# Performance work log

Measured on AMD Instinct MI355X. Metric: run time of the kernel, lower is better.

Reference implementation:

```python
import jax, jax.numpy as jnp
import numpy as np

B, N, DIM_X, DIM_E = 16, 2048, 512, 64


def setup_inputs() -> dict:
    key = jax.random.key(0)
    kx, ke, k0, k1, k2, k3 = jax.random.split(key, 6)
    s = lambda fan_in: 1.0 / np.sqrt(fan_in)
    return {
        "x": jax.random.normal(kx, (B, N, DIM_X), dtype=jnp.float32),
        "e": jax.random.normal(ke, (N, DIM_E), dtype=jnp.float32),
        # nn.Linear weights: shape [out_features, in_features], U(-1/sqrt(in), 1/sqrt(in))
        "W0": jax.random.uniform(k0, (DIM_X, DIM_X), jnp.float32, -s(DIM_X), s(DIM_X)),  # W_Q_W_KT
        "W1": jax.random.uniform(k1, (DIM_E, DIM_X), jnp.float32, -s(DIM_X), s(DIM_X)),  # Wx_Q_We_KT
        "W2": jax.random.uniform(k2, (DIM_X, DIM_E), jnp.float32, -s(DIM_E), s(DIM_E)),  # We_Q_Wx_KT
        "W3": jax.random.uniform(k3, (DIM_E, DIM_E), jnp.float32, -s(DIM_E), s(DIM_E)),  # We_Q_We_KT
    }


def reference(x, e, W0, W1, W2, W3):
    # causal_temporal_map='lower_triangle': weight <- relu(triu(weight, 1))
    W0m = jax.nn.relu(jnp.triu(W0, 1))
    # attn0 = (x @ W0m.T) @ x^T over time axis t   -> [b, n, m]
    attn0 = jnp.einsum("bnt,bmt->bnm", x @ W0m.T, x)
    # e is shared across batch (repeat); keep it 2D and broadcast
    attn1 = jnp.einsum("bne,me->bnm", x @ W1.T, e)        # Wx_Q_We_KT(x) . e
    attn2 = jnp.einsum("nt,bmt->bnm", e @ W2.T, x)        # We_Q_Wx_KT(e) . x
    attn3 = jnp.einsum("ne,me->nm", e @ W3.T, e)          # We_Q_We_KT(e) . e, batch-shared
    attn = attn0 + attn1 + attn2 + attn3[None]            # dropout p=0.0 -> identity
    # v = x.clone(); out = attn @ v
    out = jnp.einsum("bnm,bmt->bnt", attn, x)
    return out
```

## Files before the change

### kernel.cpp

```cpp
#include <hip/hip_runtime.h>
#include <hip/hip_bf16.h>


typedef __attribute__((ext_vector_type(8))) short s16x8;
typedef __attribute__((ext_vector_type(4))) short s16x4;
typedef __attribute__((ext_vector_type(4))) float f32x4;

__device__ __forceinline__ unsigned short f2bf(float f) {
  union { float f; unsigned u; } v; v.f = f;
  unsigned r = v.u + 0x7fff + ((v.u >> 16) & 1);
  return (unsigned short)(r >> 16);
}

template<int TM, int TN, int GX, int GY, int OUT_F32>
__global__ __launch_bounds__(256) void gemm_nt(
    const unsigned short* __restrict__ A, long sAb, int lda,
    const unsigned short* __restrict__ B, long sBb, int ldb,
    void* __restrict__ Cptr, long sCb, int ldc,
    int K)
{
  constexpr int TK = 64;
  constexpr int WM = TM / 2, WN = TN / 2;
  constexpr int AM = WM / 16, AN = WN / 16;
  constexpr int ACH = TM / 8;
  constexpr int BCH = TN / 8;
  constexpr int NBLK = GX * GY;

  __shared__ unsigned short As[2][TM * TK];
  __shared__ unsigned short Bs[2][TN * TK];

  const int bid  = blockIdx.x;
  const int xcd  = bid & 7;
  const int slot = bid >> 3;
  const int bz   = xcd + 8 * (slot / NBLK);
  const int tix  = slot % NBLK;
  const int m0   = (tix % GX) * TM;
  const int n0   = (tix / GX) * TN;

  const unsigned short* Ab = A + (long)bz * sAb;
  const unsigned short* Bb = B + (long)bz * sBb;

  const int tid  = threadIdx.x;
  const int lane = tid & 63;
  const int wave = tid >> 6;
  const int wm = (wave >> 1) * WM;
  const int wn = (wave & 1) * WN;
  const int fr = lane & 15;
  const int fg = lane >> 4;
  const int fx = fr & 7;

  const int srow = lane >> 3;
  const int scol = (((lane & 7) ^ (lane >> 3)) & 7) * 8;

  f32x4 acc[AM][AN];
#pragma unroll
  for (int i = 0; i < AM; i++)
#pragma unroll
    for (int j = 0; j < AN; j++) acc[i][j] = (f32x4)(0.f);

  auto stage = [&](int buf, int k0) {
#pragma unroll
    for (int i = 0; i < ACH / 4; i++) {
      const int c = wave * (ACH / 4) + i;
      __builtin_amdgcn_global_load_lds(
          (const __attribute__((address_space(1))) unsigned*)
              (Ab + (long)(m0 + c * 8 + srow) * lda + k0 + scol),
          (__attribute__((address_space(3))) unsigned*)(&As[buf][c * 512]),
          16, 0, 0);
    }
#pragma unroll
    for (int i = 0; i < BCH / 4; i++) {
      const int c = wave * (BCH / 4) + i;
      __builtin_amdgcn_global_load_lds(
          (const __attribute__((address_space(1))) unsigned*)
              (Bb + (long)(n0 + c * 8 + srow) * ldb + k0 + scol),
          (__attribute__((address_space(3))) unsigned*)(&Bs[buf][c * 512]),
          16, 0, 0);
    }
  };

  const int NT = K / TK;
  stage(0, 0);
  __syncthreads();

  for (int t = 0; t < NT; ++t) {
    const int cur = t & 1;
    if (t + 1 < NT) stage(cur ^ 1, (t + 1) * TK);

    const unsigned short* Ac = &As[cur][0];
    const unsigned short* Bc = &Bs[cur][0];
#pragma unroll
    for (int ks = 0; ks < 2; ks++) {
      s16x8 av[AM], bv[AN];
#pragma unroll
      for (int mt = 0; mt < AM; mt++)
        av[mt] = *(const s16x8*)
            &Ac[(wm + mt * 16 + fr) * TK + (((ks * 4 + fg) ^ fx) * 8)];
#pragma unroll
      for (int nt = 0; nt < AN; nt++)
        bv[nt] = *(const s16x8*)
            &Bc[(wn + nt * 16 + fr) * TK + (((ks * 4 + fg) ^ fx) * 8)];
#pragma unroll
      for (int mt = 0; mt < AM; mt++)
#pragma unroll
        for (int nt = 0; nt < AN; nt++)
          acc[mt][nt] = __builtin_amdgcn_mfma_f32_16x16x32_bf16(
              av[mt], bv[nt], acc[mt][nt], 0, 0, 0);
    }
    __syncthreads();
  }

  if (OUT_F32) {
    float* C = (float*)Cptr + (long)bz * sCb;
#pragma unroll
    for (int mt = 0; mt < AM; mt++) {
      const int row = m0 + wm + mt * 16 + fg * 4;
#pragma unroll
      for (int nt = 0; nt < AN; nt++) {
        const int col = n0 + wn + nt * 16 + fr;
#pragma unroll
        for (int j = 0; j < 4; j++)
          C[(long)(row + j) * ldc + col] = acc[mt][nt][j];
      }
    }
  } else {
    unsigned short* C = (unsigned short*)Cptr + (long)bz * sCb;
#pragma unroll
    for (int mt = 0; mt < AM; mt++) {
      const int row = m0 + wm + mt * 16 + fg * 4;
#pragma unroll
      for (int nt = 0; nt < AN; nt++) {
        const int col = n0 + wn + nt * 16 + fr;
#pragma unroll
        for (int j = 0; j < 4; j++)
          C[(long)(row + j) * ldc + col] = f2bf(acc[mt][nt][j]);
      }
    }
  }
}

__global__ __launch_bounds__(256) void convert_x(
    const float* __restrict__ x,
    unsigned short* __restrict__ XeT, unsigned short* __restrict__ Xe)
{
  const int b  = blockIdx.z;
  const int k0 = blockIdx.x * 128;
  const int f0 = blockIdx.y * 128;
  const int lane = threadIdx.x & 63;
  const int w    = threadIdx.x >> 6;
  const int fg = lane & 15;
  const int kg = w * 4 + (lane >> 4);
  const int kk = k0 + kg * 8;
  const int ff = f0 + fg * 8;

  unsigned short h[8][8];
#pragma unroll
  for (int j = 0; j < 8; ++j) {
    const float* src = &x[((long)b * 2048 + kk + j) * 512 + ff];
    float4 a = *(const float4*)src;
    float4 c = *(const float4*)(src + 4);
    h[j][0] = f2bf(a.x); h[j][1] = f2bf(a.y);
    h[j][2] = f2bf(a.z); h[j][3] = f2bf(a.w);
    h[j][4] = f2bf(c.x); h[j][5] = f2bf(c.y);
    h[j][6] = f2bf(c.z); h[j][7] = f2bf(c.w);
  }
  if (Xe) {
#pragma unroll
    for (int j = 0; j < 8; ++j) {
      s16x8 o;
#pragma unroll
      for (int q = 0; q < 8; ++q) o[q] = h[j][q];
      *(s16x8*)&Xe[((long)b * 2048 + kk + j) * 576 + ff] = o;
    }
  }
#pragma unroll
  for (int r = 0; r < 8; ++r) {
    s16x8 o;
#pragma unroll
    for (int q = 0; q < 8; ++q) o[q] = h[q][r];
    *(s16x8*)&XeT[((long)b * 576 + ff + r) * 2048 + kk] = o;
  }
}

__global__ __launch_bounds__(256) void convert_e(
    const float* __restrict__ e,
    unsigned short* __restrict__ XeT, unsigned short* __restrict__ Xe)
{
  const int b  = blockIdx.y;
  const int k0 = blockIdx.x * 256;
  const int lane = threadIdx.x & 63;
  const int w    = threadIdx.x >> 6;
  const int fg = lane & 7;
  const int kg = w * 8 + (lane >> 3);
  const int kk = k0 + kg * 8;
  const int ff = fg * 8;

  unsigned short h[8][8];
#pragma unroll
  for (int j = 0; j < 8; ++j) {
    const float* src = &e[(long)(kk + j) * 64 + ff];
    float4 a = *(const float4*)src;
    float4 c = *(const float4*)(src + 4);
    h[j][0] = f2bf(a.x); h[j][1] = f2bf(a.y);
    h[j][2] = f2bf(a.z); h[j][3] = f2bf(a.w);
    h[j][4] = f2bf(c.x); h[j][5] = f2bf(c.y);
    h[j][6] = f2bf(c.z); h[j][7] = f2bf(c.w);
  }
  if (Xe) {
#pragma unroll
    for (int j = 0; j < 8; ++j) {
      s16x8 o;
#pragma unroll
      for (int q = 0; q < 8; ++q) o[q] = h[j][q];
      *(s16x8*)&Xe[((long)b * 2048 + kk + j) * 576 + 512 + ff] = o;
    }
  }
#pragma unroll
  for (int r = 0; r < 8; ++r) {
    s16x8 o;
#pragma unroll
    for (int q = 0; q < 8; ++q) o[q] = h[q][r];
    *(s16x8*)&XeT[((long)b * 576 + 512 + ff + r) * 2048 + kk] = o;
  }
}

__global__ __launch_bounds__(256) void convert_xe(
    const float* __restrict__ x, const float* __restrict__ e,
    unsigned short* __restrict__ Xe)
{
  long g = (long)blockIdx.x * 256 + threadIdx.x;
  int  c4 = (int)(g % 144);
  long bn = g / 144;
  int  n  = (int)(bn % 2048);
  int  f  = c4 * 4;
  float4 v = (f < 512) ? *(const float4*)&x[bn * 512 + f]
                       : *(const float4*)&e[(long)n * 64 + (f - 512)];
  s16x4 o; o[0] = f2bf(v.x); o[1] = f2bf(v.y); o[2] = f2bf(v.z); o[3] = f2bf(v.w);
  *(s16x4*)&Xe[bn * 576 + f] = o;
}

__global__ __launch_bounds__(256) void build_wb(
    const float* __restrict__ W0, const float* __restrict__ W1,
    const float* __restrict__ W2, const float* __restrict__ W3,
    unsigned short* __restrict__ Wb)
{
  __shared__ float tw[32][33];
  const int m0 = blockIdx.x * 32;
  const int k0 = blockIdx.y * 32;
  const int r  = threadIdx.x >> 3;
  const int c4 = (threadIdx.x & 7) * 4;

  const int k = k0 + r;
  float4 v;
  if (m0 < 512) {
    if (k0 < 512) v = *(const float4*)&W0[k * 512 + m0 + c4];
    else          v = *(const float4*)&W1[(k - 512) * 512 + m0 + c4];
  } else {
    if (k0 < 512) v = *(const float4*)&W2[k * 64 + (m0 - 512) + c4];
    else          v = *(const float4*)&W3[(k - 512) * 64 + (m0 - 512) + c4];
  }
  tw[r][c4 + 0] = v.x; tw[r][c4 + 1] = v.y; tw[r][c4 + 2] = v.z; tw[r][c4 + 3] = v.w;
  __syncthreads();

  const int m = m0 + r;
  const bool tri = (m0 < 512) && (k0 < 512);
  s16x4 o;
#pragma unroll
  for (int j = 0; j < 4; ++j) {
    const int kk = k0 + c4 + j;
    float val = tw[c4 + j][r];
    if (tri) val = (m > kk) ? fmaxf(val, 0.f) : 0.f;
    o[j] = f2bf(val);
  }
  *(s16x4*)&Wb[m * 576 + k0 + c4] = o;
}

extern "C" void kernel_launch(void* const* d_in, const int* in_sizes, int n_in,
                              void* d_out, int out_size, void* d_ws, size_t ws_size,
                              hipStream_t stream) {
  const float* x  = (const float*)d_in[0];
  const float* e  = (const float*)d_in[1];
  const float* W0 = (const float*)d_in[2];
  const float* W1 = (const float*)d_in[3];
  const float* W2 = (const float*)d_in[4];
  const float* W3 = (const float*)d_in[5];
  float* out = (float*)d_out;

  const size_t SZ_XeT = (size_t)16 * 576 * 2048 * 2;
  const size_t SZ_CT  = (size_t)16 * 512 * 576 * 2;
  const size_t SZ_DT  = SZ_CT;
  const size_t SZ_WB  = (size_t)576 * 576 * 2;

  char* p = (char*)d_ws;
  unsigned short* XeT = (unsigned short*)p;  p += SZ_XeT;
  unsigned short* CT  = (unsigned short*)p;  p += SZ_CT;
  unsigned short* DT  = (unsigned short*)p;  p += SZ_DT;
  unsigned short* Wb  = (unsigned short*)p;  p += SZ_WB;
  const size_t base = SZ_XeT + SZ_CT + SZ_DT + SZ_WB;
  if (ws_size < base) return;
  const bool roomy = ws_size >= base + SZ_XeT;
  unsigned short* Xe = roomy ? (unsigned short*)p : XeT;

  build_wb<<<dim3(18, 18), 256, 0, stream>>>(W0, W1, W2, W3, Wb);
  convert_x<<<dim3(16, 4, 16), 256, 0, stream>>>(x, XeT, roomy ? Xe : nullptr);
  convert_e<<<dim3(8, 16), 256, 0, stream>>>(e, XeT, roomy ? Xe : nullptr);

  gemm_nt<64, 96, 8, 6, 0><<<768, 256, 0, stream>>>(
      XeT, (long)576 * 2048, 2048,
      XeT, (long)576 * 2048, 2048,
      CT,  (long)512 * 576, 576, 2048);

  if (!roomy)
    convert_xe<<<18432, 256, 0, stream>>>(x, e, Xe);

  gemm_nt<64, 96, 8, 6, 0><<<768, 256, 0, stream>>>(
      CT, (long)512 * 576, 576,
      Wb, 0L, 576,
      DT, (long)512 * 576, 576, 576);

  gemm_nt<128, 128, 16, 4, 1><<<1024, 256, 0, stream>>>(
      Xe, (long)2048 * 576, 576,
      DT, (long)512 * 576, 576,
      out, (long)2048 * 512, 512, 576);
}
```

Measured before the change: 97.96 us.

## Exploit Gram-matrix symmetry in first GEMM and split x/e operands in final GEMM

The first GEMM now computes the full 576x576 Gram matrix of [x;e] over time, but only its lower-triangular 64x64 tiles, using a triangular block index. A new mirror kernel then copies the transposed lower tiles into the rows the next GEMM reads. The final GEMM no longer needs a concatenated 576-wide Xe buffer: it reads separate bf16 x and e buffers and switches source pointer partway through K. This cuts roughly a third of the largest GEMM's MMA work and removes the interleaved Xe copy, at the cost of an extra mirror launch and a serial loop for tile index decoding.

New measurement: 100.3 us. +2.4%, slower.

```diff
diff --git a/kernel.cpp b/kernel.cpp
--- a/kernel.cpp
+++ b/kernel.cpp
@@ -12,9 +12,10 @@
   return (unsigned short)(r >> 16);
 }
 
-template<int TM, int TN, int GX, int GY, int OUT_F32>
+template<int TM, int TN, int GX, int GY, int OUT_F32, int TRI, int KSW>
 __global__ __launch_bounds__(256) void gemm_nt(
     const unsigned short* __restrict__ A, long sAb, int lda,
+    const unsigned short* __restrict__ A2, int lda2,
     const unsigned short* __restrict__ B, long sBb, int ldb,
     void* __restrict__ Cptr, long sCb, int ldc,
     int K)
@@ -24,7 +25,7 @@
   constexpr int AM = WM / 16, AN = WN / 16;
   constexpr int ACH = TM / 8;
   constexpr int BCH = TN / 8;
-  constexpr int NBLK = GX * GY;
+  constexpr int NBLK = TRI ? (GX * (GX + 1)) / 2 : GX * GY;
 
   __shared__ unsigned short As[2][TM * TK];
   __shared__ unsigned short Bs[2][TN * TK];
@@ -34,8 +35,14 @@
   const int slot = bid >> 3;
   const int bz   = xcd + 8 * (slot / NBLK);
   const int tix  = slot % NBLK;
-  const int m0   = (tix % GX) * TM;
-  const int n0   = (tix / GX) * TN;
+  int m0, n0;
+  if (TRI) {
+    int ti = 0, rem = tix;
+    while (rem >= ti + 1) { rem -= ti + 1; ++ti; }
+    m0 = ti * TM; n0 = rem * TN;
+  } else {
+    m0 = (tix % GX) * TM; n0 = (tix / GX) * TN;
+  }
 
   const unsigned short* Ab = A + (long)bz * sAb;
   const unsigned short* Bb = B + (long)bz * sBb;
@@ -58,13 +65,18 @@
 #pragma unroll
     for (int j = 0; j < AN; j++) acc[i][j] = (f32x4)(0.f);
 
-  auto stage = [&](int buf, int k0) {
+  auto stage = [&](int buf, int t) {
+    const int k0 = t * TK;
+    const unsigned short* asrc;
+    int asl;
+    if (KSW >= 0 && t >= KSW) { asrc = A2 + (k0 - KSW * TK); asl = lda2; }
+    else                      { asrc = Ab + k0;              asl = lda;  }
 #pragma unroll
     for (int i = 0; i < ACH / 4; i++) {
       const int c = wave * (ACH / 4) + i;
       __builtin_amdgcn_global_load_lds(
           (const __attribute__((address_space(1))) unsigned*)
-              (Ab + (long)(m0 + c * 8 + srow) * lda + k0 + scol),
+              (asrc + (long)(m0 + c * 8 + srow) * asl + scol),
           (__attribute__((address_space(3))) unsigned*)(&As[buf][c * 512]),
           16, 0, 0);
     }
@@ -85,7 +97,7 @@
 
   for (int t = 0; t < NT; ++t) {
     const int cur = t & 1;
-    if (t + 1 < NT) stage(cur ^ 1, (t + 1) * TK);
+    if (t + 1 < NT) stage(cur ^ 1, t + 1);
 
     const unsigned short* Ac = &As[cur][0];
     const unsigned short* Bc = &Bs[cur][0];
@@ -139,9 +151,40 @@
   }
 }
 
+__global__ __launch_bounds__(256) void mirror_g(unsigned short* __restrict__ G)
+{
+  const int it = blockIdx.x;
+  const int jt = blockIdx.y;
+  if (jt < it) return;
+  const long S = (long)576 * 576;
+  unsigned short* Gb = G + (long)blockIdx.z * S;
+  const int i0 = it * 32, j0 = jt * 32;
+  const int r  = threadIdx.x >> 3;
+  const int c4 = (threadIdx.x & 7) * 4;
+
+  __shared__ unsigned short t[32][36];
+  s16x4 v = *(const s16x4*)&Gb[(long)(j0 + r) * 576 + i0 + c4];
+#pragma unroll
+  for (int q = 0; q < 4; ++q) t[r][c4 + q] = v[q];
+  __syncthreads();
+
+  if (it == jt) {
+#pragma unroll
+    for (int q = 0; q < 4; ++q) {
+      const int j = j0 + c4 + q, i = i0 + r;
+      if (j > i) Gb[(long)i * 576 + j] = t[c4 + q][r];
+    }
+  } else {
+    s16x4 o;
+#pragma unroll
+    for (int q = 0; q < 4; ++q) o[q] = t[c4 + q][r];
+    *(s16x4*)&Gb[(long)(i0 + r) * 576 + j0 + c4] = o;
+  }
+}
+
 __global__ __launch_bounds__(256) void convert_x(
     const float* __restrict__ x,
-    unsigned short* __restrict__ XeT, unsigned short* __restrict__ Xe)
+    unsigned short* __restrict__ XeT, unsigned short* __restrict__ Xb)
 {
   const int b  = blockIdx.z;
   const int k0 = blockIdx.x * 128;
@@ -164,14 +207,12 @@
     h[j][4] = f2bf(c.x); h[j][5] = f2bf(c.y);
     h[j][6] = f2bf(c.z); h[j][7] = f2bf(c.w);
   }
-  if (Xe) {
-#pragma unroll
-    for (int j = 0; j < 8; ++j) {
-      s16x8 o;
-#pragma unroll
-      for (int q = 0; q < 8; ++q) o[q] = h[j][q];
-      *(s16x8*)&Xe[((long)b * 2048 + kk + j) * 576 + ff] = o;
-    }
+#pragma unroll
+  for (int j = 0; j < 8; ++j) {
+    s16x8 o;
+#pragma unroll
+    for (int q = 0; q < 8; ++q) o[q] = h[j][q];
+    *(s16x8*)&Xb[((long)b * 2048 + kk + j) * 512 + ff] = o;
   }
 #pragma unroll
   for (int r = 0; r < 8; ++r) {
@@ -184,7 +225,7 @@
 
 __global__ __launch_bounds__(256) void convert_e(
     const float* __restrict__ e,
-    unsigned short* __restrict__ XeT, unsigned short* __restrict__ Xe)
+    unsigned short* __restrict__ XeT, unsigned short* __restrict__ eb)
 {
   const int b  = blockIdx.y;
   const int k0 = blockIdx.x * 256;
@@ -206,13 +247,13 @@
     h[j][4] = f2bf(c.x); h[j][5] = f2bf(c.y);
     h[j][6] = f2bf(c.z); h[j][7] = f2bf(c.w);
   }
-  if (Xe) {
+  if (b == 0) {
 #pragma unroll
     for (int j = 0; j < 8; ++j) {
       s16x8 o;
 #pragma unroll
       for (int q = 0; q < 8; ++q) o[q] = h[j][q];
-      *(s16x8*)&Xe[((long)b * 2048 + kk + j) * 576 + 512 + ff] = o;
+      *(s16x8*)&eb[(long)(kk + j) * 64 + ff] = o;
     }
   }
 #pragma unroll
@@ -222,21 +263,6 @@
     for (int q = 0; q < 8; ++q) o[q] = h[q][r];
     *(s16x8*)&XeT[((long)b * 576 + 512 + ff + r) * 2048 + kk] = o;
   }
-}
-
-__global__ __launch_bounds__(256) void convert_xe(
-    const float* __restrict__ x, const float* __restrict__ e,
-    unsigned short* __restrict__ Xe)
-{
-  long g = (long)blockIdx.x * 256 + threadIdx.x;
-  int  c4 = (int)(g % 144);
-  long bn = g / 144;
-  int  n  = (int)(bn % 2048);
-  int  f  = c4 * 4;
-  float4 v = (f < 512) ? *(const float4*)&x[bn * 512 + f]
-                       : *(const float4*)&e[(long)n * 64 + (f - 512)];
-  s16x4 o; o[0] = f2bf(v.x); o[1] = f2bf(v.y); o[2] = f2bf(v.z); o[3] = f2bf(v.w);
-  *(s16x4*)&Xe[bn * 576 + f] = o;
 }
 
 __global__ __launch_bounds__(256) void build_wb(
@@ -287,39 +313,40 @@
   float* out = (float*)d_out;
 
   const size_t SZ_XeT = (size_t)16 * 576 * 2048 * 2;
-  const size_t SZ_CT  = (size_t)16 * 512 * 576 * 2;
-  const size_t SZ_DT  = SZ_CT;
+  const size_t SZ_G   = (size_t)16 * 576 * 576 * 2;
+  const size_t SZ_DT  = (size_t)16 * 512 * 576 * 2;
   const size_t SZ_WB  = (size_t)576 * 576 * 2;
+  const size_t SZ_XB  = (size_t)16 * 2048 * 512 * 2;
+  const size_t SZ_EB  = (size_t)2048 * 64 * 2;
 
   char* p = (char*)d_ws;
   unsigned short* XeT = (unsigned short*)p;  p += SZ_XeT;
-  unsigned short* CT  = (unsigned short*)p;  p += SZ_CT;
+  unsigned short* G   = (unsigned short*)p;  p += SZ_G;
   unsigned short* DT  = (unsigned short*)p;  p += SZ_DT;
   unsigned short* Wb  = (unsigned short*)p;  p += SZ_WB;
-  const size_t base = SZ_XeT + SZ_CT + SZ_DT + SZ_WB;
+  unsigned short* Xb  = (unsigned short*)p;  p += SZ_XB;
+  unsigned short* eb  = (unsigned short*)p;  p += SZ_EB;
+  const size_t base = SZ_XeT + SZ_G + SZ_DT + SZ_WB + SZ_XB + SZ_EB;
   if (ws_size < base) return;
-  const bool roomy = ws_size >= base + SZ_XeT;
-  unsigned short* Xe = roomy ? (unsigned short*)p : XeT;
 
   build_wb<<<dim3(18, 18), 256, 0, stream>>>(W0, W1, W2, W3, Wb);
-  convert_x<<<dim3(16, 4, 16), 256, 0, stream>>>(x, XeT, roomy ? Xe : nullptr);
-  convert_e<<<dim3(8, 16), 256, 0, stream>>>(e, XeT, roomy ? Xe : nullptr);
-
-  gemm_nt<64, 96, 8, 6, 0><<<768, 256, 0, stream>>>(
+  convert_x<<<dim3(16, 4, 16), 256, 0, stream>>>(x, XeT, Xb);
+  convert_e<<<dim3(8, 16), 256, 0, stream>>>(e, XeT, eb);
+
+  gemm_nt<64, 64, 9, 0, 0, 1, -1><<<720, 256, 0, stream>>>(
+      XeT, (long)576 * 2048, 2048, nullptr, 0,
       XeT, (long)576 * 2048, 2048,
-      XeT, (long)576 * 2048, 2048,
-      CT,  (long)512 * 576, 576, 2048);
-
-  if (!roomy)
-    convert_xe<<<18432, 256, 0, stream>>>(x, e, Xe);
-
-  gemm_nt<64, 96, 8, 6, 0><<<768, 256, 0, stream>>>(
-      CT, (long)512 * 576, 576,
+      G,   (long)576 * 576, 576, 2048);
+
+  mirror_g<<<dim3(16, 18, 16), 256, 0, stream>>>(G);
+
+  gemm_nt<64, 96, 8, 6, 0, 0, -1><<<768, 256, 0, stream>>>(
+      G,  (long)576 * 576, 576, nullptr, 0,
       Wb, 0L, 576,
       DT, (long)512 * 576, 576, 576);
 
-  gemm_nt<128, 128, 16, 4, 1><<<1024, 256, 0, stream>>>(
-      Xe, (long)2048 * 576, 576,
+  gemm_nt<128, 128, 16, 4, 1, 0, 8><<<1024, 256, 0, stream>>>(
+      Xb, (long)2048 * 512, 512, eb, 64,
       DT, (long)512 * 576, 576,
       out, (long)2048 * 512, 512, 576);
 }
```
